# Kernel optimization log

Measured on AMD Instinct MI355X. Metric: run time of the kernel, lower is better.

## Reference

```python
import jax, jax.numpy as jnp
import numpy as np

TEMP = 0.07
N, D = 8192, 256
NUM_CLASSES = 512


def setup_inputs() -> dict:
    key = jax.random.key(0)
    k1, k2 = jax.random.split(key)
    features = jax.random.normal(k1, (N, D), dtype=jnp.float32)
    labels = jax.random.randint(k2, (N,), 0, NUM_CLASSES, dtype=jnp.int64)
    return {"features": features, "labels": labels}


def reference(features, labels):
    n = features.shape[0]
    # L2 normalize rows (torch F.normalize, eps=1e-12)
    norm = jnp.sqrt(jnp.sum(features * features, axis=1, keepdims=True))
    f = features / jnp.maximum(norm, 1e-12)
    # [N, N] cosine similarities scaled by temperature
    logits = jnp.matmul(f, f.T) / TEMP
    # positive-pair mask (same label), excluding self
    mask = (labels[:, None] == labels[None, :]).astype(logits.dtype)
    logits_mask = 1.0 - jnp.eye(n, dtype=logits.dtype)
    mask = mask * logits_mask
    # denominator excludes self-similarity
    exp_logits = jnp.exp(logits) * logits_mask
    log_prob = logits - jnp.log(jnp.sum(exp_logits, axis=1, keepdims=True) + 1e-6)
    mean_log_prob_pos = jnp.sum(mask * log_prob, axis=1) / jnp.clip(jnp.sum(mask, axis=1), 1.0, None)
    return -jnp.mean(mean_log_prob_pos)
```

## Files before the change

### kernel.cpp

```cpp
#include <hip/hip_runtime.h>
#include <hip/hip_bf16.h>

#define N 8192
#define D 256
#define NCLS 512
#define INV_TEMP 14.285714285714286f
#define C1 20.609929155f
#define JSPLIT 16

typedef __bf16 bf16x8 __attribute__((ext_vector_type(8)));
typedef float f32x4 __attribute__((ext_vector_type(4)));

static __device__ __forceinline__ unsigned short f2bf(float x) {
    unsigned int u = __float_as_uint(x);
    u = (u + 0x7fffu + ((u >> 16) & 1u)) >> 16;
    return (unsigned short)u;
}
static __device__ __forceinline__ float bf2f(unsigned short b) {
    return __uint_as_float(((unsigned int)b) << 16);
}

__global__ __launch_bounds__(256) void norm_kernel(const float* __restrict__ feat,
                                                   __bf16* __restrict__ fb,
                                                   float* __restrict__ rowDS) {
    const int gt = blockIdx.x * 256 + (int)threadIdx.x;
    if (gt < 2 * N) rowDS[gt] = 0.0f;
    const int row = gt >> 6;
    const int lane = threadIdx.x & 63;
    if (row >= N) return;
    float4 v = reinterpret_cast<const float4*>(feat + (size_t)row * D)[lane];
    float ss = v.x * v.x + v.y * v.y + v.z * v.z + v.w * v.w;
#pragma unroll
    for (int m = 1; m < 64; m <<= 1) ss += __shfl_xor(ss, m);
    const float inv = 1.0f / fmaxf(sqrtf(ss), 1e-12f);
    ushort4 o;
    o.x = f2bf(v.x * inv); o.y = f2bf(v.y * inv);
    o.z = f2bf(v.z * inv); o.w = f2bf(v.w * inv);
    reinterpret_cast<ushort4*>(fb + (size_t)row * D)[lane] = o;
}

__global__ __launch_bounds__(256, 2) void supcon_main(const __bf16* __restrict__ fb,
                                                      const int* __restrict__ labels,
                                                      float* __restrict__ rowD,
                                                      float* __restrict__ rowS) {
    __shared__ __align__(1024) char lds[32768];
    const int lane = threadIdx.x & 63;
    const int w = threadIdx.x >> 6;
    const int l4 = lane & 15;
    const int lh = lane >> 4;
    const int wrow = blockIdx.x * 256 + w * 64;
    const int jbase = blockIdx.y * (N / JSPLIT);
    const char* fbb = (const char*)fb;

    bf16x8 a[4][8];
#pragma unroll
    for (int mf = 0; mf < 4; ++mf)
#pragma unroll
        for (int k = 0; k < 8; ++k)
            a[mf][k] = *reinterpret_cast<const bf16x8*>(
                fbb + (size_t)(wrow + mf * 16 + l4) * 512 + k * 64 + lh * 16);

    int labi[4][4];
#pragma unroll
    for (int mf = 0; mf < 4; ++mf)
#pragma unroll
        for (int r = 0; r < 4; ++r) labi[mf][r] = labels[wrow + mf * 16 + lh * 4 + r];

    const int s7 = l4 & 7;
    const int lhx = lh ^ (s7 & 3);
    const int b2v = (s7 >> 2) & 1;
    const int rb_common = l4 * 512 + lhx * 16;

    auto stage = [&](int bufsel, int jb) {
#pragma unroll
        for (int r = 0; r < 4; ++r) {
            const int gidx = r * 256 + (int)threadIdx.x;
            const int row = gidx >> 5, h = gidx & 31;
            const char* src = fbb + (size_t)(jb + row) * 512 + ((h ^ (row & 7)) * 16);
            char* dst = lds + bufsel * 16384 + r * 4096 + w * 1024;
            __builtin_amdgcn_global_load_lds(
                (const __attribute__((address_space(1))) void*)src,
                (__attribute__((address_space(3))) void*)dst, 16, 0, 0);
        }
    };

    float dsum[4][4] = {};
    float ssum[4][4] = {};

    const int njt = (N / JSPLIT) / 32;
    int cur = 0;
    stage(0, jbase);
    __syncthreads();

    for (int jt = 0; jt < njt; ++jt) {
        const int jb = jbase + jt * 32;
        if (jt + 1 < njt) stage(cur ^ 1, jb + 32);

        int labj[2];
        labj[0] = labels[jb + l4];
        labj[1] = labels[jb + 16 + l4];

        const char* bb = lds + cur * 16384 + rb_common;
        const char* rb0 = bb + b2v * 64;
        const char* rb1 = bb + 64 - b2v * 64;

        f32x4 c[4][2] = {};
#pragma unroll
        for (int q = 0; q < 4; ++q) {
            bf16x8 b00 = *(const bf16x8*)(rb0 + q * 128);
            bf16x8 b01 = *(const bf16x8*)(rb0 + 8192 + q * 128);
            bf16x8 b10 = *(const bf16x8*)(rb1 + q * 128);
            bf16x8 b11 = *(const bf16x8*)(rb1 + 8192 + q * 128);
#pragma unroll
            for (int mf = 0; mf < 4; ++mf) {
                c[mf][0] = __builtin_amdgcn_mfma_f32_16x16x32_bf16(a[mf][2 * q], b00, c[mf][0], 0, 0, 0);
                c[mf][1] = __builtin_amdgcn_mfma_f32_16x16x32_bf16(a[mf][2 * q], b01, c[mf][1], 0, 0, 0);
                c[mf][0] = __builtin_amdgcn_mfma_f32_16x16x32_bf16(a[mf][2 * q + 1], b10, c[mf][0], 0, 0, 0);
                c[mf][1] = __builtin_amdgcn_mfma_f32_16x16x32_bf16(a[mf][2 * q + 1], b11, c[mf][1], 0, 0, 0);
            }
        }

#pragma unroll
        for (int mf = 0; mf < 4; ++mf) {
#pragma unroll
            for (int cf = 0; cf < 2; ++cf) {
                const f32x4 cc = c[mf][cf];
                if (wrow + mf * 16 == jb + cf * 16) {
#pragma unroll
                    for (int r = 0; r < 4; ++r) {
                        const float t = cc[r];
                        const bool diag = (l4 == lh * 4 + r);
                        dsum[mf][r] += diag ? 0.0f : __builtin_amdgcn_exp2f(t * C1);
                        const bool pos = (labi[mf][r] == labj[cf]) && !diag;
                        ssum[mf][r] += pos ? t : 0.0f;
                    }
                } else {
#pragma unroll
                    for (int r = 0; r < 4; ++r) {
                        const float t = cc[r];
                        dsum[mf][r] += __builtin_amdgcn_exp2f(t * C1);
                        ssum[mf][r] += (labi[mf][r] == labj[cf]) ? t : 0.0f;
                    }
                }
            }
        }
        __syncthreads();
        cur ^= 1;
    }

#pragma unroll
    for (int mf = 0; mf < 4; ++mf) {
#pragma unroll
        for (int r = 0; r < 4; ++r) {
            float v1 = dsum[mf][r], v2 = ssum[mf][r];
#pragma unroll
            for (int m = 1; m < 16; m <<= 1) {
                v1 += __shfl_xor(v1, m);
                v2 += __shfl_xor(v2, m);
            }
            if (l4 == 0) {
                const int rg = wrow + mf * 16 + lh * 4 + r;
                atomicAdd(&rowD[rg], v1);
                atomicAdd(&rowS[rg], v2 * INV_TEMP);
            }
        }
    }
}

__global__ __launch_bounds__(256) void finalize_kernel(const int* __restrict__ labels,
                                                       const float* __restrict__ rowD,
                                                       const float* __restrict__ rowS,
                                                       float* __restrict__ out) {
    __shared__ int hist[NCLS];
    __shared__ float red[4];
    for (int i = threadIdx.x; i < NCLS; i += 256) hist[i] = 0;
    __syncthreads();
    for (int i = threadIdx.x; i < N; i += 256) atomicAdd(&hist[labels[i]], 1);
    __syncthreads();
    float local = 0.0f;
    for (int r = threadIdx.x; r < N; r += 256) {
        const float c = (float)(hist[labels[r]] - 1);
        local += (rowS[r] - c * __logf(rowD[r] + 1e-6f)) / fmaxf(c, 1.0f);
    }
#pragma unroll
    for (int m = 1; m < 64; m <<= 1) local += __shfl_xor(local, m);
    if ((threadIdx.x & 63) == 0) red[threadIdx.x >> 6] = local;
    __syncthreads();
    if (threadIdx.x == 0) out[0] = -(red[0] + red[1] + red[2] + red[3]) / (float)N;
}

extern "C" void kernel_launch(void* const* d_in, const int* in_sizes, int n_in,
                              void* d_out, int out_size, void* d_ws, size_t ws_size,
                              hipStream_t stream) {
    const float* feat = (const float*)d_in[0];
    const int* labels = (const int*)d_in[1];

    __bf16* fb = (__bf16*)d_ws;
    float* rowD = (float*)((char*)d_ws + (size_t)N * D * 2);
    float* rowS = rowD + N;

    norm_kernel<<<N / 4, 256, 0, stream>>>(feat, fb, rowD);
    dim3 grid(N / 256, JSPLIT);
    supcon_main<<<grid, 256, 0, stream>>>(fb, labels, rowD, rowS);
    finalize_kernel<<<1, 256, 0, stream>>>(labels, rowD, rowS, (float*)d_out);
}
```

Before: 117.6 us.

## Exploit Gram matrix symmetry to compute only upper-triangular tiles

Because f·fᵀ is symmetric, each block now handles only upper-triangular tiles. It adds every off-diagonal tile's exp and positive-label sums to both the row and the column accumulators, which roughly halves the MFMA and exp work. The grid becomes a flattened triangular enumeration of 1056 blocks, each covering a 256x128 tile, and block indices are decoded with a small loop. The trade-offs are extra column shuffles and atomics, a load imbalance where diagonal blocks skip part of their work, and shorter per-block loops with less pipelining.

```diff
diff --git a/kernel.cpp b/kernel.cpp
--- a/kernel.cpp
+++ b/kernel.cpp
@@ -6,7 +6,6 @@
 #define NCLS 512
 #define INV_TEMP 14.285714285714286f
 #define C1 20.609929155f
-#define JSPLIT 16
 
 typedef __bf16 bf16x8 __attribute__((ext_vector_type(8)));
 typedef float f32x4 __attribute__((ext_vector_type(4)));
@@ -15,9 +14,6 @@
     unsigned int u = __float_as_uint(x);
     u = (u + 0x7fffu + ((u >> 16) & 1u)) >> 16;
     return (unsigned short)u;
-}
-static __device__ __forceinline__ float bf2f(unsigned short b) {
-    return __uint_as_float(((unsigned int)b) << 16);
 }
 
 __global__ __launch_bounds__(256) void norm_kernel(const float* __restrict__ feat,
@@ -48,8 +44,13 @@
     const int w = threadIdx.x >> 6;
     const int l4 = lane & 15;
     const int lh = lane >> 4;
-    const int wrow = blockIdx.x * 256 + w * 64;
-    const int jbase = blockIdx.y * (N / JSPLIT);
+
+    int I = 0, rem = (int)blockIdx.x;
+    while (rem >= 64 - 2 * I) { rem -= 64 - 2 * I; ++I; }
+    const int brow = I * 256;
+    const int wrow = brow + w * 64;
+    const int cbase = brow + rem * 128;
+
     const char* fbb = (const char*)fb;
 
     bf16x8 a[4][8];
@@ -86,60 +87,74 @@
 
     float dsum[4][4] = {};
     float ssum[4][4] = {};
-
-    const int njt = (N / JSPLIT) / 32;
+    float colD[8] = {};
+    float colS[8] = {};
+
+    const int njt = 4;
     int cur = 0;
-    stage(0, jbase);
+    stage(0, cbase);
     __syncthreads();
 
     for (int jt = 0; jt < njt; ++jt) {
-        const int jb = jbase + jt * 32;
+        const int jb = cbase + jt * 32;
         if (jt + 1 < njt) stage(cur ^ 1, jb + 32);
 
-        int labj[2];
-        labj[0] = labels[jb + l4];
-        labj[1] = labels[jb + 16 + l4];
-
-        const char* bb = lds + cur * 16384 + rb_common;
-        const char* rb0 = bb + b2v * 64;
-        const char* rb1 = bb + 64 - b2v * 64;
-
-        f32x4 c[4][2] = {};
-#pragma unroll
-        for (int q = 0; q < 4; ++q) {
-            bf16x8 b00 = *(const bf16x8*)(rb0 + q * 128);
-            bf16x8 b01 = *(const bf16x8*)(rb0 + 8192 + q * 128);
-            bf16x8 b10 = *(const bf16x8*)(rb1 + q * 128);
-            bf16x8 b11 = *(const bf16x8*)(rb1 + 8192 + q * 128);
+        if (jb + 32 > wrow) {
+            int labj[2];
+            labj[0] = labels[jb + l4];
+            labj[1] = labels[jb + 16 + l4];
+
+            const char* bb = lds + cur * 16384 + rb_common;
+            const char* rb0 = bb + b2v * 64;
+            const char* rb1 = bb + 64 - b2v * 64;
+
+            f32x4 c[4][2] = {};
+#pragma unroll
+            for (int q = 0; q < 4; ++q) {
+                bf16x8 b00 = *(const bf16x8*)(rb0 + q * 128);
+                bf16x8 b01 = *(const bf16x8*)(rb0 + 8192 + q * 128);
+                bf16x8 b10 = *(const bf16x8*)(rb1 + q * 128);
+                bf16x8 b11 = *(const bf16x8*)(rb1 + 8192 + q * 128);
+#pragma unroll
+                for (int mf = 0; mf < 4; ++mf) {
+                    c[mf][0] = __builtin_amdgcn_mfma_f32_16x16x32_bf16(a[mf][2 * q], b00, c[mf][0], 0, 0, 0);
+                    c[mf][1] = __builtin_amdgcn_mfma_f32_16x16x32_bf16(a[mf][2 * q], b01, c[mf][1], 0, 0, 0);
+                    c[mf][0] = __builtin_amdgcn_mfma_f32_16x16x32_bf16(a[mf][2 * q + 1], b10, c[mf][0], 0, 0, 0);
+                    c[mf][1] = __builtin_amdgcn_mfma_f32_16x16x32_bf16(a[mf][2 * q + 1], b11, c[mf][1], 0, 0, 0);
+                }
+            }
+
 #pragma unroll
             for (int mf = 0; mf < 4; ++mf) {
-                c[mf][0] = __builtin_amdgcn_mfma_f32_16x16x32_bf16(a[mf][2 * q], b00, c[mf][0], 0, 0, 0);
-                c[mf][1] = __builtin_amdgcn_mfma_f32_16x16x32_bf16(a[mf][2 * q], b01, c[mf][1], 0, 0, 0);
-                c[mf][0] = __builtin_amdgcn_mfma_f32_16x16x32_bf16(a[mf][2 * q + 1], b10, c[mf][0], 0, 0, 0);
-                c[mf][1] = __builtin_amdgcn_mfma_f32_16x16x32_bf16(a[mf][2 * q + 1], b11, c[mf][1], 0, 0, 0);
-            }
-        }
-
-#pragma unroll
-        for (int mf = 0; mf < 4; ++mf) {
-#pragma unroll
-            for (int cf = 0; cf < 2; ++cf) {
-                const f32x4 cc = c[mf][cf];
-                if (wrow + mf * 16 == jb + cf * 16) {
-#pragma unroll
-                    for (int r = 0; r < 4; ++r) {
-                        const float t = cc[r];
-                        const bool diag = (l4 == lh * 4 + r);
-                        dsum[mf][r] += diag ? 0.0f : __builtin_amdgcn_exp2f(t * C1);
-                        const bool pos = (labi[mf][r] == labj[cf]) && !diag;
-                        ssum[mf][r] += pos ? t : 0.0f;
-                    }
-                } else {
-#pragma unroll
-                    for (int r = 0; r < 4; ++r) {
-                        const float t = cc[r];
-                        dsum[mf][r] += __builtin_amdgcn_exp2f(t * C1);
-                        ssum[mf][r] += (labi[mf][r] == labj[cf]) ? t : 0.0f;
+#pragma unroll
+                for (int cf = 0; cf < 2; ++cf) {
+                    const int r0 = wrow + mf * 16;
+                    const int c0 = jb + cf * 16;
+                    if (c0 < r0) continue;
+                    const f32x4 cc = c[mf][cf];
+                    if (c0 == r0) {
+#pragma unroll
+                        for (int r = 0; r < 4; ++r) {
+                            const float t = cc[r];
+                            const bool diag = (l4 == lh * 4 + r);
+                            dsum[mf][r] += diag ? 0.0f : __builtin_amdgcn_exp2f(t * C1);
+                            const bool pos = (labi[mf][r] == labj[cf]) && !diag;
+                            ssum[mf][r] += pos ? t : 0.0f;
+                        }
+                    } else {
+                        float es = 0.0f, ts = 0.0f;
+#pragma unroll
+                        for (int r = 0; r < 4; ++r) {
+                            const float t = cc[r];
+                            const float e = __builtin_amdgcn_exp2f(t * C1);
+                            dsum[mf][r] += e;
+                            const float tm = (labi[mf][r] == labj[cf]) ? t : 0.0f;
+                            ssum[mf][r] += tm;
+                            es += e;
+                            ts += tm;
+                        }
+                        colD[jt * 2 + cf] += es;
+                        colS[jt * 2 + cf] += ts;
                     }
                 }
             }
@@ -163,6 +178,18 @@
                 atomicAdd(&rowD[rg], v1);
                 atomicAdd(&rowS[rg], v2 * INV_TEMP);
             }
+        }
+    }
+
+#pragma unroll
+    for (int e = 0; e < 8; ++e) {
+        float v1 = colD[e], v2 = colS[e];
+        v1 += __shfl_xor(v1, 16); v1 += __shfl_xor(v1, 32);
+        v2 += __shfl_xor(v2, 16); v2 += __shfl_xor(v2, 32);
+        if (lh == 0) {
+            const int col = cbase + (e >> 1) * 32 + (e & 1) * 16 + l4;
+            atomicAdd(&rowD[col], v1);
+            atomicAdd(&rowS[col], v2 * INV_TEMP);
         }
     }
 }
@@ -200,7 +227,6 @@
     float* rowS = rowD + N;
 
     norm_kernel<<<N / 4, 256, 0, stream>>>(feat, fb, rowD);
-    dim3 grid(N / 256, JSPLIT);
-    supcon_main<<<grid, 256, 0, stream>>>(fb, labels, rowD, rowS);
+    supcon_main<<<1056, 256, 0, stream>>>(fb, labels, rowD, rowS);
     finalize_kernel<<<1, 256, 0, stream>>>(labels, rowD, rowS, (float*)d_out);
 }
```

Measured after the change: 142.2 us. 1.21x slower.
